# Optimization experiments

Hardware: AMD Instinct MI355X
Metric: run time of the kernel (lower is better)

The kernel has to match this reference:

```python
import jax, jax.numpy as jnp
from jax import lax
import numpy as np

N, C_IN, C_OUT, H, W, DS = 32, 16, 1, 128, 128, 5
NC = C_OUT * C_IN  # channels fed to DUBlock convs (= out_nc*nc_d[0])


def autocorr(x, ds):
    """x:(N,C,H,W) -> xtx_raw:(N,C,C,2ds-1,2ds-1).
    xtx_raw[n,i,j,u,v] = sum_{h,w} x[n,i,h,w] * xpad[n,j,u+h,v+w]  (zero pad ds-1),
    matching torch cal_xtx (sample-wise conv3d of x with itself)."""
    n, c, h, w = x.shape
    p = ds - 1
    xp = jnp.pad(x, ((0, 0), (0, 0), (p, p), (p, p)))
    rows = []
    for u in range(2 * ds - 1):
        cols = [jnp.einsum('nihw,njhw->nij', x,
                           lax.slice(xp, (0, 0, u, v), (n, c, u + h, v + w)))
                for v in range(2 * ds - 1)]
        rows.append(jnp.stack(cols, axis=-1))
    return jnp.stack(rows, axis=-2)  # (N,C,C,K,K), K=2ds-1


def crosscorr(x, y, ds):
    """x:(N,Ci,H,W), y:(N,Co,H,W) -> xty:(N,Co,Ci,ds,ds)  (torch cal_xty, pad=(ds-1)//2)."""
    n, c, h, w = x.shape
    p = (ds - 1) // 2
    xp = jnp.pad(x, ((0, 0), (0, 0), (p, p), (p, p)))
    rows = []
    for u in range(ds):
        cols = [jnp.einsum('nohw,njhw->noj', y,
                           lax.slice(xp, (0, 0, u, v), (n, c, u + h, v + w)))
                for v in range(ds)]
        rows.append(jnp.stack(cols, axis=-1))
    return jnp.stack(rows, axis=-2)  # (N,Co,Ci,ds,ds)


def assemble_Q(R, ds):
    """Block-Toeplitz assembly. Equivalent to torch's unfold + flip + index permutation:
    Q[n,(i,p,q),(j,oi,oj)] = R[n,i,j, ds-1+oi-p, ds-1+oj-q]."""
    n, c = R.shape[0], R.shape[1]
    r = jnp.arange(ds)
    idx = (ds - 1) + r[None, :] - r[:, None]  # idx[p,o] = ds-1+o-p in [0, 2ds-2]
    Q6 = R[:, :, :, idx[:, None, :, None], idx[None, :, None, :]]  # (N,i,j,p,q,oi,oj)
    return jnp.transpose(Q6, (0, 1, 3, 4, 2, 5, 6)).reshape(n, c * ds * ds, c * ds * ds)


def dsb(x, d, y, alpha, reg):
    """DSBlock: regularized normal equations + batched SPD solve.
    x:(N,Ci,H,W), d:(N,Co,Ci,ds,ds), y:(N,Co,H,W), alpha:(N,1,1,1), reg:(1,)"""
    n, ci, h, w = x.shape
    co, ds = d.shape[1], d.shape[-1]
    Q = assemble_Q(autocorr(x, ds), ds)                               # (N, ci*ds^2, ci*ds^2)
    P = crosscorr(x, y, ds).reshape(n, co, -1).transpose(0, 2, 1)      # (N, ci*ds^2, co)
    a = alpha.reshape(n, 1, 1) * (h * w) * reg / (ds * ds * ci)        # (N,1,1)
    m = Q.shape[1]
    Q = Q + a * jnp.eye(m, dtype=Q.dtype)
    P = P + a * d.reshape(n, co, -1).transpose(0, 2, 1)
    # torch uses cholesky + cholesky_solve on SPD Q; jnp.linalg.solve computes the
    # same solution (and its vjp matches the custom CholeskySolve backward for symmetric Q).
    D = jnp.linalg.solve(Q, P)                                         # (N, ci*ds^2, co)
    return D.reshape(n, ci, ds, ds, co).transpose(0, 4, 1, 2, 3)       # (N,Co,Ci,ds,ds)


def conv3x3(x, wgt, b):
    o = lax.conv_general_dilated(x, wgt, (1, 1), ((1, 1), (1, 1)),
                                 dimension_numbers=('NCHW', 'OIHW', 'NCHW'))
    return o + b[None, :, None, None]


def dblock_fwd(x1, x2, d, y1, y2, alpha, beta, reg,
               w1, b1, w2, b2, w3, b3, w4, b4, w5, b5, w6, b6):
    d = dsb(x1, d, y1, alpha, reg)
    d = dsb(x2, d, y2, alpha, reg)
    n, co, ci, ds = d.shape[0], d.shape[1], d.shape[2], d.shape[3]
    bmap = jnp.broadcast_to(1.0 / jnp.sqrt(beta), (n, 1, ds, ds))      # (1/beta.sqrt()).repeat
    h0 = jnp.concatenate([d.reshape(n, co * ci, ds, ds), bmap], axis=1)
    # DUBlock
    t = jax.nn.relu(conv3x3(jax.nn.relu(conv3x3(h0, w1, b1)), w2, b2))
    t = jax.nn.relu(conv3x3(jax.nn.relu(conv3x3(t, w3, b3)), w4, b4))
    t = conv3x3(jax.nn.relu(conv3x3(t, w5, b5)), w6, b6) + h0[:, :-1]
    return t.reshape(n, co, ci, ds, ds)


def setup_inputs() -> dict:
    key = jax.random.key(0)
    ks = jax.random.split(key, 24)
    inp = {
        'x1': jax.random.normal(ks[0], (N, C_IN, H, W), jnp.float32),
        'x2': jax.random.normal(ks[1], (N, C_IN, H, W), jnp.float32),
        'd': jax.random.normal(ks[2], (N, C_OUT, C_IN, DS, DS), jnp.float32),
        'y1': jax.random.normal(ks[3], (N, C_OUT, H, W), jnp.float32),
        'y2': jax.random.normal(ks[4], (N, C_OUT, H, W), jnp.float32),
        'alpha': jax.random.uniform(ks[5], (N, 1, 1, 1), jnp.float32),
        'beta': jax.random.uniform(ks[6], (N, 1, 1, 1), jnp.float32),
        'reg': jnp.ones((1,), jnp.float32),
    }
    cins = [NC + 1, NC, NC, NC, NC, NC]
    for i in range(6):
        inp['w%d' % (i + 1)] = 0.05 * jax.random.normal(ks[7 + i], (NC, cins[i], 3, 3), jnp.float32)
        inp['b%d' % (i + 1)] = jnp.zeros((NC,), jnp.float32)
    return inp


def reference(x1, x2, d, y1, y2, alpha, beta, reg,
              w1, b1, w2, b2, w3, b3, w4, b4, w5, b5, w6, b6):
    return dblock_fwd(x1, x2, d, y1, y2, alpha, beta, reg,
                      w1, b1, w2, b2, w3, b3, w4, b4, w5, b5, w6, b6)
```

## Files before the change

### kernel.cpp

```cpp
#include <hip/hip_runtime.h>
#include <hip/hip_bf16.h>

constexpr int NS   = 32;
constexpr int C    = 16;
constexpr int H    = 128;
constexpr int W    = 128;
constexpr int DS   = 5;
constexpr int M    = C * DS * DS;
constexpr int NLAG = 81;

typedef short short8 __attribute__((ext_vector_type(8)));
typedef float f32x4 __attribute__((ext_vector_type(4)));

constexpr int CH_U    = 152;
constexpr int SLOT_U  = 16 * CH_U;
constexpr int SLOT_B  = SLOT_U * 2;
constexpr int RING_B  = 16 * SLOT_B;

constexpr int WREP_F  = 6 * 144 * 20 + 6 * 16;
constexpr int WREP_CH = WREP_F * 4 / 16;

constexpr int PVP = 29;

__device__ __forceinline__ unsigned int pk_bf16(float a, float b) {
    union { __hip_bfloat162 h; unsigned int u; } cv;
    cv.h = __float22bfloat162_rn(make_float2(a, b));
    return cv.u;
}

__device__ __forceinline__ void gl_lds16(const void* g, void* l) {
    __builtin_amdgcn_global_load_lds(
        (const __attribute__((address_space(1))) unsigned int*)g,
        (__attribute__((address_space(3))) unsigned int*)l, 16, 0, 0);
}

__global__ __launch_bounds__(256, 1)
void prep_kernel(const float* __restrict__ x1, const float* __restrict__ x2,
                 const float* __restrict__ y1, const float* __restrict__ y2,
                 float* __restrict__ P1, float* __restrict__ P2,
                 const float* __restrict__ w1, const float* __restrict__ b1,
                 const float* __restrict__ w2, const float* __restrict__ b2,
                 const float* __restrict__ w3, const float* __restrict__ b3,
                 const float* __restrict__ w4, const float* __restrict__ b4,
                 const float* __restrict__ w5, const float* __restrict__ b5,
                 const float* __restrict__ w6, const float* __restrict__ b6,
                 float* __restrict__ wrep)
{
    const int b = blockIdx.x, tid = threadIdx.x;
    if (b < 1024) {
        const int n = b & 31, j = (b >> 5) & 15, zi = b >> 9;
        const float* x = zi ? x2 : x1;
        const float* y = zi ? y2 : y1;
        float* P       = zi ? P2 : P1;

        const float* yn = y + (size_t)n * H * W;
        const float* xc = x + ((size_t)n * C + j) * H * W;

        const int wg = tid & 31, slab = tid >> 5;
        const int r0 = slab * 16;

        float acc[25];
#pragma unroll
        for (int l = 0; l < 25; ++l) acc[l] = 0.f;

        float4 yw[5];
#pragma unroll
        for (int u = 0; u < 5; ++u) {
            const int t = r0 + 1 - u;
            yw[u] = (t >= 0) ? *(const float4*)(yn + (size_t)t * W + wg * 4)
                             : make_float4(0.f, 0.f, 0.f, 0.f);
        }

#pragma unroll 4
        for (int rr = 0; rr < 16; ++rr) {
            const int r = r0 + rr;
#pragma unroll
            for (int u = 4; u >= 1; --u) yw[u] = yw[u - 1];
            const int tnew = r + 2;
            yw[0] = (tnew < H) ? *(const float4*)(yn + (size_t)tnew * W + wg * 4)
                               : make_float4(0.f, 0.f, 0.f, 0.f);

            const float* xr = xc + (size_t)r * W + wg * 4;
            float w12[12];
            float4 t4 = (wg > 0) ? *(const float4*)(xr - 4) : make_float4(0, 0, 0, 0);
            w12[0] = t4.x; w12[1] = t4.y; w12[2] = t4.z; w12[3] = t4.w;
            t4 = *(const float4*)(xr);
            w12[4] = t4.x; w12[5] = t4.y; w12[6] = t4.z; w12[7] = t4.w;
            t4 = (wg < 31) ? *(const float4*)(xr + 4) : make_float4(0, 0, 0, 0);
            w12[8] = t4.x; w12[9] = t4.y; w12[10] = t4.z; w12[11] = t4.w;

#pragma unroll
            for (int u = 0; u < 5; ++u) {
#pragma unroll
                for (int v = 0; v < 5; ++v)
                    acc[u * 5 + v] += yw[u].x * w12[2 + v] + yw[u].y * w12[3 + v] +
                                      yw[u].z * w12[4 + v] + yw[u].w * w12[5 + v];
            }
        }

        __shared__ float red[4][25];
        const int lane = tid & 63, wv = tid >> 6;
#pragma unroll
        for (int l = 0; l < 25; ++l) {
            float v = acc[l];
#pragma unroll
            for (int off = 32; off; off >>= 1) v += __shfl_down(v, off);
            if (lane == 0) red[wv][l] = v;
        }
        __syncthreads();
        if (tid < 25)
            P[((size_t)n * C + j) * 25 + tid] = red[0][tid] + red[1][tid] + red[2][tid] + red[3][tid];
        return;
    }
    const float* wsl[6] = {w1, w2, w3, w4, w5, w6};
    const float* bsl[6] = {b1, b2, b3, b4, b5, b6};
#pragma unroll
    for (int l = 0; l < 6; ++l) {
        const int cin = (l == 0) ? 17 : 16;
        const float* ws = wsl[l];
        for (int f = tid; f < 16 * cin * 9; f += 256) {
            const int o = f / (cin * 9);
            const int rm = f - o * cin * 9;
            const int ci = rm / 9, kk = rm - ci * 9;
            wrep[l * 2880 + (o * 9 + kk) * 20 + ci] = ws[f];
        }
        if (tid < 16) wrep[17280 + l * 16 + tid] = bsl[l][tid];
    }
}

__device__ __forceinline__ void stage4(const float* __restrict__ xn,
                                       char* sm, int row0, int tid)
{
    const int pair = tid >> 3;
    const int sub  = tid & 7;
    const int rr   = pair >> 4;
    const int ch   = pair & 15;
    const int row  = row0 + rr;
    const float4* src = (const float4*)(xn + ((size_t)ch * H + row) * W + sub * 16);
    const float4 a = src[0], b = src[1], c = src[2], d = src[3];
    unsigned short* dst = (unsigned short*)sm + (row & 15) * SLOT_U + ch * CH_U + 8 + sub * 16;
    *(uint4*)(dst)     = make_uint4(pk_bf16(a.x, a.y), pk_bf16(a.z, a.w),
                                    pk_bf16(b.x, b.y), pk_bf16(b.z, b.w));
    *(uint4*)(dst + 8) = make_uint4(pk_bf16(c.x, c.y), pk_bf16(c.z, c.w),
                                    pk_bf16(d.x, d.y), pk_bf16(d.z, d.w));
}

template<int P0, int P1>
__device__ __forceinline__ void autocorr_body(const float* __restrict__ xn,
                                              float* __restrict__ Rn,
                                              char* sm, int tid)
{
    constexpr int U0 = P0 / 9;
    constexpr int U1 = (P1 - 1) / 9;
    constexpr int NB = U1 - U0 + 1;
    constexpr int NP = P1 - P0;
    constexpr int SLOT_Q = SLOT_B / 16;

    unsigned short* ring = (unsigned short*)sm;
    const int lane = tid & 63;
    const int wid  = tid >> 6;
    const int q    = lane >> 4;
    const int mi   = lane & 15;
    const int rh   = wid & 3;
    const int chh  = wid >> 2;

    f32x4 acc[NP];
#pragma unroll
    for (int l = 0; l < NP; ++l) acc[l] = (f32x4){0.f, 0.f, 0.f, 0.f};

    for (int f = tid; f < 4 * SLOT_Q; f += 512)
        ((uint4*)sm)[(12 + f / SLOT_Q) * SLOT_Q + (f % SLOT_Q)] = make_uint4(0, 0, 0, 0);
    if (tid < 192) {
        const int slot = tid >> 4, ch = tid & 15;
        unsigned short* sb = ring + slot * SLOT_U + ch * CH_U;
        *(uint4*)(sb)       = make_uint4(0u, 0u, 0u, 0u);
        *(uint4*)(sb + 136) = make_uint4(0u, 0u, 0u, 0u);
        *(uint4*)(sb + 144) = make_uint4(0u, 0u, 0u, 0u);
    }
    stage4(xn, sm, 0, tid);
    stage4(xn, sm, 4, tid);
    __syncthreads();

    for (int s = 0; s < H; s += 4) {
        if (s < H - 8) {
            stage4(xn, sm, s + 8, tid);
        } else {
            for (int f = tid; f < 4 * SLOT_Q; f += 512)
                ((uint4*)sm)[(((s + 8 + f / SLOT_Q) & 15)) * SLOT_Q + (f % SLOT_Q)] = make_uint4(0, 0, 0, 0);
        }

        const int r = s + rh;
        const unsigned short* rowA = ring + (r & 15) * SLOT_U + mi * CH_U;
#pragma unroll
        for (int cc = 0; cc < 2; ++cc) {
            const int w0 = (chh * 2 + cc) * 32;
            const uint4* pa = (const uint4*)(rowA + w0 + 8 * q);
            uint4 A0 = pa[0], A1 = pa[1], A2 = pa[2];
            unsigned int d[12] = {A0.x, A0.y, A0.z, A0.w, A1.x, A1.y, A1.z, A1.w,
                                  A2.x, A2.y, A2.z, A2.w};
            short8 bf[NB];
#pragma unroll
            for (int u = U0; u <= U1; ++u)
                bf[u - U0] = *(const short8*)(ring + ((r + u - 4 + 16) & 15) * SLOT_U +
                                              mi * CH_U + 8 + w0 + 8 * q);
#pragma unroll
            for (int v = 0; v < 9; ++v) {
                const int off = 12 - v;
                const int q4  = off >> 1;
                union { unsigned int u4[4]; short8 s8; } af;
                if (off & 1) {
#pragma unroll
                    for (int k2 = 0; k2 < 4; ++k2)
                        af.u4[k2] = (d[q4 + k2] >> 16) | (d[q4 + k2 + 1] << 16);
                } else {
#pragma unroll
                    for (int k2 = 0; k2 < 4; ++k2) af.u4[k2] = d[q4 + k2];
                }
#pragma unroll
                for (int u = U0; u <= U1; ++u) {
                    if (u * 9 + v >= P0 && u * 9 + v < P1)
                        acc[u * 9 + v - P0] = __builtin_amdgcn_mfma_f32_16x16x32_bf16(
                            af.s8, bf[u - U0], acc[u * 9 + v - P0], 0, 0, 0);
                }
            }
        }
        __syncthreads();
    }

    float* sred = (float*)sm;
#pragma unroll
    for (int cb = 0; cb < NP; cb += 9) {
        const int nc = (NP - cb < 9) ? (NP - cb) : 9;
        __syncthreads();
#pragma unroll
        for (int pp = 0; pp < 9; ++pp) {
            if (pp < nc) {
#pragma unroll
                for (int rg = 0; rg < 4; ++rg)
                    sred[(pp * 8 + wid) * 256 + (q * 4 + rg) * 16 + mi] = acc[cb + pp][rg];
            }
        }
        __syncthreads();
        if (tid < 256) {
#pragma unroll
            for (int pp = 0; pp < 9; ++pp) {
                if (pp < nc) {
                    float ssum = 0.f;
#pragma unroll
                    for (int w8 = 0; w8 < 8; ++w8)
                        ssum += sred[(pp * 8 + w8) * 256 + tid];
                    Rn[(size_t)tid * NLAG + P0 + cb + pp] = ssum;
                }
            }
        }
    }
}

__global__ __launch_bounds__(512, 2)
void autocorr_mfma(const float* __restrict__ x1, const float* __restrict__ x2,
                   float* __restrict__ R1, float* __restrict__ R2)
{
    __shared__ __align__(16) char sm[RING_B];
    const int b = blockIdx.x;
    const int xcd = b & 7, k = b >> 3;
    const int slice = xcd * 8 + (k >> 2);
    const int ug = k & 3;
    const int n = slice & 31, zi = slice >> 5;
    const float* xn = (zi ? x2 : x1) + (size_t)n * C * H * W;
    float* Rn = (zi ? R2 : R1) + (size_t)n * C * C * NLAG;
    switch (ug) {
        case 0:  autocorr_body< 0, 20>(xn, Rn, sm, threadIdx.x); break;
        case 1:  autocorr_body<20, 40>(xn, Rn, sm, threadIdx.x); break;
        case 2:  autocorr_body<40, 60>(xn, Rn, sm, threadIdx.x); break;
        default: autocorr_body<60, 81>(xn, Rn, sm, threadIdx.x); break;
    }
}

__device__ __forceinline__ float block_sum256(float v, float* red, int t)
{
#pragma unroll
    for (int off = 32; off; off >>= 1) v += __shfl_down(v, off);
    if ((t & 63) == 0) red[t >> 6] = v;
    __syncthreads();
    float s = red[0] + red[1] + red[2] + red[3];
    __syncthreads();
    return s;
}

__device__ __forceinline__ void cg_solve(const float (&Rreg)[81],
                                         float rhs0, float rhs1,
                                         int iters, float a, int t, bool has1,
                                         float* pv, float* ap, float* red,
                                         float& z0o, float& z1o)
{
    const int jj = t & 15;
    const int e1 = t + 256;
    float z0 = 0.f, z1 = 0.f;
    float r0 = rhs0, r1 = has1 ? rhs1 : 0.f;
    float p0 = r0, p1 = r1;
    pv[(t / 25) * PVP + (t % 25)] = p0;
    if (has1) pv[(e1 / 25) * PVP + (e1 % 25)] = p1;
    float rr = block_sum256(r0 * r0 + r1 * r1, red, t);

    for (int it = 0; it < iters; ++it) {
        float pld[25], acc[25];
        const float* pj = &pv[jj * PVP];
#pragma unroll
        for (int k = 0; k < 25; ++k) pld[k] = pj[k];
#pragma unroll
        for (int k = 0; k < 25; ++k) acc[k] = 0.f;
#pragma unroll
        for (int u = 0; u < 9; ++u) {
#pragma unroll
            for (int v = 0; v < 9; ++v) {
                const float Rv = Rreg[u * 9 + v];
#pragma unroll
                for (int c = 0; c < 5; ++c) {
                    if (c < u - 4 || c > u) continue;
                    const int aa = 4 + c - u;
#pragma unroll
                    for (int dd = 0; dd < 5; ++dd) {
                        if (dd < v - 4 || dd > v) continue;
                        const int bb = 4 + dd - v;
                        acc[aa * 5 + bb] += Rv * pld[c * 5 + dd];
                    }
                }
            }
        }
#pragma unroll
        for (int k = 0; k < 25; ++k) {
            float s2 = acc[k];
            s2 += __shfl_down(s2, 8, 16);
            s2 += __shfl_down(s2, 4, 16);
            s2 += __shfl_down(s2, 2, 16);
            s2 += __shfl_down(s2, 1, 16);
            acc[k] = s2;
        }
        if (jj == 0) {
#pragma unroll
            for (int k = 0; k < 25; ++k) ap[(t >> 4) * 25 + k] = acc[k];
        }
        __syncthreads();
        const float w0 = ap[t] + a * p0;
        const float w1 = has1 ? (ap[e1] + a * p1) : 0.f;
        const float pAp = block_sum256(p0 * w0 + p1 * w1, red, t);
        const float al  = (pAp > 1e-30f) ? rr / pAp : 0.f;
        z0 += al * p0; z1 += al * p1;
        if (it + 1 < iters) {
            r0 -= al * w0; r1 -= al * w1;
            const float rrn = block_sum256(r0 * r0 + r1 * r1, red, t);
            const float be  = (rr > 1e-30f) ? rrn / rr : 0.f;
            rr = rrn;
            p0 = r0 + be * p0; p1 = r1 + be * p1;
            pv[(t / 25) * PVP + (t % 25)] = p0;
            if (has1) pv[(e1 / 25) * PVP + (e1 % 25)] = p1;
            __syncthreads();
        }
    }
    z0o = z0; z1o = z1;
}

__device__ __forceinline__ float conv_one(const float* __restrict__ act,
                                          const float* __restrict__ wall,
                                          int l, int idx)
{
    const int o = idx / 25, pix = idx % 25, yy = pix / 5, xx = pix % 5;
    float s = wall[17280 + l * 16 + o];
#pragma unroll
    for (int ky = 0; ky < 3; ++ky) {
        const int iy = yy + ky - 1;
        if ((unsigned)iy >= 5u) continue;
#pragma unroll
        for (int kx = 0; kx < 3; ++kx) {
            const int ix = xx + kx - 1;
            if ((unsigned)ix >= 5u) continue;
            const float* ip = act + (iy * 5 + ix) * 20;
            const float* wp = wall + l * 2880 + (o * 9 + ky * 3 + kx) * 20;
            const float4 a0 = *(const float4*)(ip);
            const float4 a1 = *(const float4*)(ip + 4);
            const float4 a2 = *(const float4*)(ip + 8);
            const float4 a3 = *(const float4*)(ip + 12);
            const float4 q0 = *(const float4*)(wp);
            const float4 q1 = *(const float4*)(wp + 4);
            const float4 q2 = *(const float4*)(wp + 8);
            const float4 q3 = *(const float4*)(wp + 12);
            s += a0.x * q0.x + a0.y * q0.y + a0.z * q0.z + a0.w * q0.w
               + a1.x * q1.x + a1.y * q1.y + a1.z * q1.z + a1.w * q1.w
               + a2.x * q2.x + a2.y * q2.y + a2.z * q2.z + a2.w * q2.w
               + a3.x * q3.x + a3.y * q3.y + a3.z * q3.z + a3.w * q3.w;
            if (l == 0) s += ip[16] * wp[16];
        }
    }
    return s;
}

__global__ __launch_bounds__(256, 1)
void solve_kernel(const float* __restrict__ R1, const float* __restrict__ R2,
                  const float* __restrict__ P1, const float* __restrict__ P2,
                  const float* __restrict__ d0, const float* __restrict__ alpha,
                  const float* __restrict__ beta, const float* __restrict__ reg,
                  const float* __restrict__ wrep,
                  float* __restrict__ out)
{
    __shared__ __align__(16) float Rl[256 * NLAG];
    __shared__ float pv[16 * PVP];
    __shared__ float ap[M];
    __shared__ float red[8];
    __shared__ float h0p[25 * 20];
    __shared__ float bufA[25 * 20], bufB[25 * 20];

    const int n = blockIdx.x, t = threadIdx.x;
    const bool has1 = (t < M - 256);
    const int e1 = t + 256;
    const float a = alpha[n] * (float)(H * W) * reg[0] / (float)(DS * DS * C);

    {
        const char* g = (const char*)(R1 + (size_t)n * 256 * NLAG);
        char* l = (char*)Rl;
        for (int f = t; f < 5184; f += 256)
            gl_lds16(g + (size_t)f * 16, l + (size_t)f * 16);
    }
    const float rhs10 = P1[(size_t)n * M + t] + a * d0[(size_t)n * M + t];
    const float rhs11 = has1 ? (P1[(size_t)n * M + e1] + a * d0[(size_t)n * M + e1]) : 0.f;
    __syncthreads();

    float Rreg[81];
    {
        const float* Rrow = &Rl[t * NLAG];
#pragma unroll
        for (int i = 0; i < 81; ++i) Rreg[i] = Rrow[i];
    }
    __syncthreads();

    {
        const char* g = (const char*)(R2 + (size_t)n * 256 * NLAG);
        char* l = (char*)Rl;
        for (int f = t; f < 5184; f += 256)
            gl_lds16(g + (size_t)f * 16, l + (size_t)f * 16);
    }
    float z1a, z1b;
    cg_solve(Rreg, rhs10, rhs11, 3, a, t, has1, pv, ap, red, z1a, z1b);
    {
        const float* Rrow = &Rl[t * NLAG];
#pragma unroll
        for (int i = 0; i < 81; ++i) Rreg[i] = Rrow[i];
    }
    __syncthreads();

    {
        const char* g = (const char*)wrep;
        char* l = (char*)Rl;
        for (int f = t; f < WREP_CH; f += 256)
            gl_lds16(g + (size_t)f * 16, l + (size_t)f * 16);
    }
    const float rhs20 = P2[(size_t)n * M + t] + a * z1a;
    const float rhs21 = has1 ? (P2[(size_t)n * M + e1] + a * z1b) : 0.f;
    float z20, z21;
    cg_solve(Rreg, rhs20, rhs21, 7, a, t, has1, pv, ap, red, z20, z21);

    const float* wall = (const float*)Rl;
    h0p[(t % 25) * 20 + t / 25] = z20;
    if (has1) h0p[(e1 % 25) * 20 + e1 / 25] = z21;
    if (t < 25) h0p[t * 20 + 16] = rsqrtf(beta[n]);
    __syncthreads();

#pragma unroll
    for (int l = 0; l < 6; ++l) {
        const float* act = (l == 0) ? h0p : ((l & 1) ? bufA : bufB);
        float s0 = conv_one(act, wall, l, t);
        float s1 = has1 ? conv_one(act, wall, l, e1) : 0.f;
        if (l < 5) { s0 = fmaxf(s0, 0.f); s1 = fmaxf(s1, 0.f); }
        else {
            s0 += h0p[(t % 25) * 20 + t / 25];
            if (has1) s1 += h0p[(e1 % 25) * 20 + e1 / 25];
        }
        if (l == 5) {
            out[(size_t)n * M + t] = s0;
            if (has1) out[(size_t)n * M + e1] = s1;
        } else {
            float* dstb = (l & 1) ? bufB : bufA;
            dstb[(t % 25) * 20 + t / 25] = s0;
            if (has1) dstb[(e1 % 25) * 20 + e1 / 25] = s1;
        }
        __syncthreads();
    }
}

extern "C" void kernel_launch(void* const* d_in, const int* in_sizes, int n_in,
                              void* d_out, int out_size, void* d_ws, size_t ws_size,
                              hipStream_t stream)
{
    (void)in_sizes; (void)n_in; (void)out_size; (void)ws_size;
    const float* x1    = (const float*)d_in[0];
    const float* x2    = (const float*)d_in[1];
    const float* d0    = (const float*)d_in[2];
    const float* y1    = (const float*)d_in[3];
    const float* y2    = (const float*)d_in[4];
    const float* alpha = (const float*)d_in[5];
    const float* beta  = (const float*)d_in[6];
    const float* reg   = (const float*)d_in[7];
    const float* w1 = (const float*)d_in[8];  const float* b1 = (const float*)d_in[9];
    const float* w2 = (const float*)d_in[10]; const float* b2 = (const float*)d_in[11];
    const float* w3 = (const float*)d_in[12]; const float* b3 = (const float*)d_in[13];
    const float* w4 = (const float*)d_in[14]; const float* b4 = (const float*)d_in[15];
    const float* w5 = (const float*)d_in[16]; const float* b5 = (const float*)d_in[17];
    const float* w6 = (const float*)d_in[18]; const float* b6 = (const float*)d_in[19];
    float* out = (float*)d_out;

    char* wsb = (char*)d_ws;
    float* R1 = (float*)wsb;
    const size_t RSZ = (size_t)NS * C * C * NLAG;
    float* R2 = R1 + RSZ;
    float* P1 = R2 + RSZ;
    float* P2 = P1 + (size_t)NS * M;
    float* wrep = P2 + (size_t)NS * M;

    prep_kernel<<<1025, 256, 0, stream>>>(x1, x2, y1, y2, P1, P2,
                                          w1, b1, w2, b2, w3, b3, w4, b4,
                                          w5, b5, w6, b6, wrep);
    autocorr_mfma<<<256, 512, 0, stream>>>(x1, x2, R1, R2);
    solve_kernel<<<NS, 256, 0, stream>>>(R1, R2, P1, P2, d0, alpha, beta, reg,
                                         wrep, out);
}
```

Baseline: 256.0 us.

## Split autocorrelation over two row halves per slice and merge with atomics

The autocorrelation kernel now launches twice as many blocks, each covering 64 of the 128 image rows for one lag group, with halo rows staged for the second half. Partial sums are merged into R with atomicAdd, so R is zeroed with a memset beforehand. This raises block-level parallelism (256 to 512 blocks) to fill more CUs, at the cost of an extra memset, atomic traffic, and extra halo staging.

Result: slower. 386.5 us (+51.0%).

```diff
diff --git a/kernel.cpp b/kernel.cpp
--- a/kernel.cpp
+++ b/kernel.cpp
@@ -148,7 +148,7 @@
 template<int P0, int P1>
 __device__ __forceinline__ void autocorr_body(const float* __restrict__ xn,
                                               float* __restrict__ Rn,
-                                              char* sm, int tid)
+                                              char* sm, int tid, int rbase)
 {
     constexpr int U0 = P0 / 9;
     constexpr int U1 = (P1 - 1) / 9;
@@ -168,23 +168,36 @@
 #pragma unroll
     for (int l = 0; l < NP; ++l) acc[l] = (f32x4){0.f, 0.f, 0.f, 0.f};
 
-    for (int f = tid; f < 4 * SLOT_Q; f += 512)
-        ((uint4*)sm)[(12 + f / SLOT_Q) * SLOT_Q + (f % SLOT_Q)] = make_uint4(0, 0, 0, 0);
-    if (tid < 192) {
-        const int slot = tid >> 4, ch = tid & 15;
-        unsigned short* sb = ring + slot * SLOT_U + ch * CH_U;
-        *(uint4*)(sb)       = make_uint4(0u, 0u, 0u, 0u);
-        *(uint4*)(sb + 136) = make_uint4(0u, 0u, 0u, 0u);
-        *(uint4*)(sb + 144) = make_uint4(0u, 0u, 0u, 0u);
-    }
-    stage4(xn, sm, 0, tid);
-    stage4(xn, sm, 4, tid);
-    __syncthreads();
-
-    for (int s = 0; s < H; s += 4) {
-        if (s < H - 8) {
-            stage4(xn, sm, s + 8, tid);
-        } else {
+    if (rbase == 0) {
+        for (int f = tid; f < 4 * SLOT_Q; f += 512)
+            ((uint4*)sm)[(12 + f / SLOT_Q) * SLOT_Q + (f % SLOT_Q)] = make_uint4(0, 0, 0, 0);
+        if (tid < 192) {
+            const int slot = tid >> 4, ch = tid & 15;
+            unsigned short* sb = ring + slot * SLOT_U + ch * CH_U;
+            *(uint4*)(sb)       = make_uint4(0u, 0u, 0u, 0u);
+            *(uint4*)(sb + 136) = make_uint4(0u, 0u, 0u, 0u);
+            *(uint4*)(sb + 144) = make_uint4(0u, 0u, 0u, 0u);
+        }
+        stage4(xn, sm, 0, tid);
+        stage4(xn, sm, 4, tid);
+    } else {
+        if (tid < 256) {
+            const int slot = tid >> 4, ch = tid & 15;
+            unsigned short* sb = ring + slot * SLOT_U + ch * CH_U;
+            *(uint4*)(sb)       = make_uint4(0u, 0u, 0u, 0u);
+            *(uint4*)(sb + 136) = make_uint4(0u, 0u, 0u, 0u);
+            *(uint4*)(sb + 144) = make_uint4(0u, 0u, 0u, 0u);
+        }
+        stage4(xn, sm, 60, tid);
+        stage4(xn, sm, 64, tid);
+        stage4(xn, sm, 68, tid);
+    }
+    __syncthreads();
+
+    for (int s = 0; s < 64; s += 4) {
+        if (s <= 52 || (s == 56 && rbase == 0)) {
+            stage4(xn, sm, rbase + s + 8, tid);
+        } else if (s == 56) {
             for (int f = tid; f < 4 * SLOT_Q; f += 512)
                 ((uint4*)sm)[(((s + 8 + f / SLOT_Q) & 15)) * SLOT_Q + (f % SLOT_Q)] = make_uint4(0, 0, 0, 0);
         }
@@ -249,7 +262,7 @@
 #pragma unroll
                     for (int w8 = 0; w8 < 8; ++w8)
                         ssum += sred[(pp * 8 + w8) * 256 + tid];
-                    Rn[(size_t)tid * NLAG + P0 + cb + pp] = ssum;
+                    atomicAdd(&Rn[(size_t)tid * NLAG + P0 + cb + pp], ssum);
                 }
             }
         }
@@ -263,16 +276,19 @@
     __shared__ __align__(16) char sm[RING_B];
     const int b = blockIdx.x;
     const int xcd = b & 7, k = b >> 3;
-    const int slice = xcd * 8 + (k >> 2);
-    const int ug = k & 3;
+    const int sl_local = k >> 3;
+    const int r2 = k & 7;
+    const int half = r2 >> 2, ug = r2 & 3;
+    const int slice = xcd * 8 + sl_local;
     const int n = slice & 31, zi = slice >> 5;
+    const int rbase = half * 64;
     const float* xn = (zi ? x2 : x1) + (size_t)n * C * H * W;
     float* Rn = (zi ? R2 : R1) + (size_t)n * C * C * NLAG;
     switch (ug) {
-        case 0:  autocorr_body< 0, 20>(xn, Rn, sm, threadIdx.x); break;
-        case 1:  autocorr_body<20, 40>(xn, Rn, sm, threadIdx.x); break;
-        case 2:  autocorr_body<40, 60>(xn, Rn, sm, threadIdx.x); break;
-        default: autocorr_body<60, 81>(xn, Rn, sm, threadIdx.x); break;
+        case 0:  autocorr_body< 0, 20>(xn, Rn, sm, threadIdx.x, rbase); break;
+        case 1:  autocorr_body<20, 40>(xn, Rn, sm, threadIdx.x, rbase); break;
+        case 2:  autocorr_body<40, 60>(xn, Rn, sm, threadIdx.x, rbase); break;
+        default: autocorr_body<60, 81>(xn, Rn, sm, threadIdx.x, rbase); break;
     }
 }
 
@@ -515,10 +531,11 @@
     float* P2 = P1 + (size_t)NS * M;
     float* wrep = P2 + (size_t)NS * M;
 
+    hipMemsetAsync(R1, 0, 2 * RSZ * sizeof(float), stream);
     prep_kernel<<<1025, 256, 0, stream>>>(x1, x2, y1, y2, P1, P2,
                                           w1, b1, w2, b2, w3, b3, w4, b4,
                                           w5, b5, w6, b6, wrep);
-    autocorr_mfma<<<256, 512, 0, stream>>>(x1, x2, R1, R2);
+    autocorr_mfma<<<512, 512, 0, stream>>>(x1, x2, R1, R2);
     solve_kernel<<<NS, 256, 0, stream>>>(R1, R2, P1, P2, d0, alpha, beta, reg,
                                          wrep, out);
 }
```
